# Kernel tuning notes

Hardware: AMD Instinct MI355X
Metric: run time of the kernel (lower is better)

The kernel has to match this reference:

```python
import jax, jax.numpy as jnp
import numpy as np

NF, NLOC, NALL, NNEI = 2, 2048, 3072, 128
Q_DIM = K_DIM = V_DIM = 256
H, D = 8, 32  # num_heads, head_dim
TOTAL = H * D


def setup_inputs() -> dict:
    key = jax.random.key(0)
    ks = jax.random.split(key, 12)
    inp = {
        "q": jax.random.normal(ks[0], (NF, NLOC, Q_DIM), jnp.float32),
        "k": jax.random.normal(ks[1], (NF, NALL, K_DIM), jnp.float32),
        "v": jax.random.normal(ks[2], (NF, NALL, V_DIM), jnp.float32),
        "nlist": jax.random.randint(ks[3], (NF, NLOC, NNEI), 0, NALL, jnp.int64),
        "bias": jax.random.normal(ks[4], (NF, H, NLOC, NNEI), jnp.float32),
        # torch Linear weights: [out, in]
        "Wq": jax.random.normal(ks[5], (TOTAL, Q_DIM), jnp.float32) * 0.05,
        "Wk": jax.random.normal(ks[6], (TOTAL, K_DIM), jnp.float32) * 0.05,
        "Wv": jax.random.normal(ks[7], (TOTAL, V_DIM), jnp.float32) * 0.05,
        "Wg": jax.random.normal(ks[8], (TOTAL, Q_DIM), jnp.float32) * 0.05,
        "bg": jnp.ones((TOTAL,), jnp.float32),  # gating init: bias=1
        "Wo": jax.random.normal(ks[9], (Q_DIM, TOTAL), jnp.float32) * 0.05,
        "bo": jnp.zeros((Q_DIM,), jnp.float32),
    }
    return inp


def reference(q, k, v, nlist, bias, Wq, Wk, Wv, Wg, bg, Wo, bo):
    nf, nloc, _ = q.shape
    nnei = nlist.shape[-1]
    norm = D ** (-0.5)

    g = q @ Wg.T + bg                       # [nf, nloc, TOTAL]
    qh = (q @ Wq.T) * norm                  # [nf, nloc, TOTAL]
    kh = k @ Wk.T                           # [nf, nall, TOTAL]
    vh = v @ Wv.T                           # [nf, nall, TOTAL]

    # gather neighbors: [nf, nloc, nnei, TOTAL]
    fidx = jnp.arange(nf)[:, None, None]
    kg = kh[fidx, nlist].reshape(nf, nloc, nnei, H, D)
    vg = vh[fidx, nlist].reshape(nf, nloc, nnei, H, D)
    qh = qh.reshape(nf, nloc, H, D)

    # per-atom attention: single query vs nnei neighbors
    attn = jnp.einsum("fnhd,fnihd->fhni", qh, kg)      # [nf, H, nloc, nnei]
    attn = jax.nn.softmax(attn + bias, axis=-1)
    o = jnp.einsum("fhni,fnihd->fnhd", attn, vg)       # [nf, nloc, H, D]
    o = o.reshape(nf, nloc, TOTAL)

    o = jax.nn.sigmoid(g) * o
    return o @ Wo.T + bo
```

## Files before the change

### kernel.cpp

```cpp
#include <hip/hip_runtime.h>

#define NF_   2
#define NLOC_ 2048
#define NALL_ 3072
#define NNEI_ 128
#define H_    8
#define D_    32
#define CH_   256

typedef __attribute__((ext_vector_type(8))) short  short8v;
typedef __attribute__((ext_vector_type(8))) unsigned short ushort8v;
typedef __attribute__((ext_vector_type(4))) float  floatx4;

__device__ __forceinline__ unsigned short f2bf(float x) {
  unsigned u = __float_as_uint(x);
  unsigned r = u + 0x7fff + ((u >> 16) & 1);
  return (unsigned short)(r >> 16);
}
__device__ __forceinline__ float bf2f(unsigned short h) {
  return __uint_as_float(((unsigned)h) << 16);
}

__device__ __forceinline__ void cvt_store(unsigned short* hp, unsigned short* lp,
                                          float4 u, float4 v) {
  ushort8v hv, lv;
  hv[0] = f2bf(u.x); lv[0] = f2bf(u.x - bf2f(hv[0]));
  hv[1] = f2bf(u.y); lv[1] = f2bf(u.y - bf2f(hv[1]));
  hv[2] = f2bf(u.z); lv[2] = f2bf(u.z - bf2f(hv[2]));
  hv[3] = f2bf(u.w); lv[3] = f2bf(u.w - bf2f(hv[3]));
  hv[4] = f2bf(v.x); lv[4] = f2bf(v.x - bf2f(hv[4]));
  hv[5] = f2bf(v.y); lv[5] = f2bf(v.y - bf2f(hv[5]));
  hv[6] = f2bf(v.z); lv[6] = f2bf(v.z - bf2f(hv[6]));
  hv[7] = f2bf(v.w); lv[7] = f2bf(v.w - bf2f(hv[7]));
  *(ushort8v*)hp = hv;
  *(ushort8v*)lp = lv;
}

__device__ __forceinline__ void gemm_mfma(
    const float* __restrict__ A, const float* __restrict__ W,
    const float* __restrict__ bvec, float* __restrict__ C,
    int M, int mode,
    unsigned short (*Ah)[40], unsigned short (*Al)[40],
    unsigned short (*Wh)[40], unsigned short (*Wl)[40]) {
  const int t  = threadIdx.x;
  const int m0 = blockIdx.y * 128;
  if (m0 >= M) return;
  const int n0 = blockIdx.x * 128;

  const int lane = t & 63;
  const int wv   = t >> 6;
  const int wr   = wv >> 1;
  const int wc   = wv & 1;
  const int l15  = lane & 15;
  const int ko   = (lane >> 4) * 8;

  const int sr = t >> 1;
  const int sk = (t & 1) * 16;

  floatx4 acc[4][4] = {};

  for (int k0 = 0; k0 < 256; k0 += 32) {
    const float* Ap = A + (size_t)(m0 + sr) * 256 + k0 + sk;
    const float* Wp = W + (size_t)(n0 + sr) * 256 + k0 + sk;
    const float4 a0 = *(const float4*)(Ap + 0);
    const float4 a1 = *(const float4*)(Ap + 4);
    const float4 a2 = *(const float4*)(Ap + 8);
    const float4 a3 = *(const float4*)(Ap + 12);
    const float4 w0 = *(const float4*)(Wp + 0);
    const float4 w1 = *(const float4*)(Wp + 4);
    const float4 w2 = *(const float4*)(Wp + 8);
    const float4 w3 = *(const float4*)(Wp + 12);
    __syncthreads();
    cvt_store(&Ah[sr][sk + 0], &Al[sr][sk + 0], a0, a1);
    cvt_store(&Ah[sr][sk + 8], &Al[sr][sk + 8], a2, a3);
    cvt_store(&Wh[sr][sk + 0], &Wl[sr][sk + 0], w0, w1);
    cvt_store(&Wh[sr][sk + 8], &Wl[sr][sk + 8], w2, w3);
    __syncthreads();

    short8v afh[4], afl[4], bfh[4], bfl[4];
#pragma unroll
    for (int mi = 0; mi < 4; ++mi) {
      const int rr = wr * 64 + mi * 16 + l15;
      afh[mi] = *(const short8v*)&Ah[rr][ko];
      afl[mi] = *(const short8v*)&Al[rr][ko];
    }
#pragma unroll
    for (int ni = 0; ni < 4; ++ni) {
      const int rr = wc * 64 + ni * 16 + l15;
      bfh[ni] = *(const short8v*)&Wh[rr][ko];
      bfl[ni] = *(const short8v*)&Wl[rr][ko];
    }
#pragma unroll
    for (int mi = 0; mi < 4; ++mi)
#pragma unroll
      for (int ni = 0; ni < 4; ++ni) {
        acc[mi][ni] = __builtin_amdgcn_mfma_f32_16x16x32_bf16(
            afh[mi], bfh[ni], acc[mi][ni], 0, 0, 0);
        acc[mi][ni] = __builtin_amdgcn_mfma_f32_16x16x32_bf16(
            afh[mi], bfl[ni], acc[mi][ni], 0, 0, 0);
        acc[mi][ni] = __builtin_amdgcn_mfma_f32_16x16x32_bf16(
            afl[mi], bfh[ni], acc[mi][ni], 0, 0, 0);
      }
  }

  const float norm = 0.17677669529663687f;
#pragma unroll
  for (int mi = 0; mi < 4; ++mi)
#pragma unroll
    for (int ni = 0; ni < 4; ++ni) {
      const int col = n0 + wc * 64 + ni * 16 + l15;
      const float bv = (mode == 1 || mode == 3) ? bvec[col] : 0.f;
#pragma unroll
      for (int r = 0; r < 4; ++r) {
        const int row = m0 + wr * 64 + mi * 16 + (lane >> 4) * 4 + r;
        float vv = acc[mi][ni][r];
        if (mode == 0)      vv *= norm;
        else if (mode == 1) vv = 1.f / (1.f + __expf(-(vv + bv)));
        else if (mode == 3) vv += bv;
        C[(size_t)row * 256 + col] = vv;
      }
    }
}

__global__ __launch_bounds__(256, 2) void proj_kernel(
    const float* __restrict__ q, const float* __restrict__ k, const float* __restrict__ v,
    const float* __restrict__ Wq, const float* __restrict__ Wg,
    const float* __restrict__ Wk, const float* __restrict__ Wv,
    const float* __restrict__ bg,
    float* __restrict__ qh, float* __restrict__ gs,
    float* __restrict__ kh, float* __restrict__ vh) {
  __shared__ unsigned short Ah[128][40], Al[128][40], Wh[128][40], Wl[128][40];
  switch (blockIdx.z) {
    case 0:  gemm_mfma(q, Wq, nullptr, qh, NF_ * NLOC_, 0, Ah, Al, Wh, Wl); break;
    case 1:  gemm_mfma(q, Wg, bg,      gs, NF_ * NLOC_, 1, Ah, Al, Wh, Wl); break;
    case 2:  gemm_mfma(k, Wk, nullptr, kh, NF_ * NALL_, 2, Ah, Al, Wh, Wl); break;
    default: gemm_mfma(v, Wv, nullptr, vh, NF_ * NALL_, 2, Ah, Al, Wh, Wl); break;
  }
}

__global__ __launch_bounds__(256, 2) void out_gemm_kernel(
    const float* __restrict__ x, const float* __restrict__ Wo,
    const float* __restrict__ bo, float* __restrict__ out) {
  __shared__ unsigned short Ah[128][40], Al[128][40], Wh[128][40], Wl[128][40];
  gemm_mfma(x, Wo, bo, out, NF_ * NLOC_, 3, Ah, Al, Wh, Wl);
}

__global__ __launch_bounds__(256, 2) void attn_kernel(
    const float* __restrict__ qh, const float* __restrict__ gs,
    const float* __restrict__ kh, const float* __restrict__ vh,
    const void* __restrict__ nlist, const float* __restrict__ bias,
    float* __restrict__ x) {
  __shared__ float q_s[CH_];
  __shared__ int   jn[NNEI_];
  __shared__ float p[H_][NNEI_ + 4];
  __shared__ float K_s[32][256];

  const int t   = threadIdx.x;
  const int bid = blockIdx.x;
  const int f   = bid >> 11;
  const int n   = bid & (NLOC_ - 1);
  const size_t row = (size_t)bid;

  q_s[t] = qh[row * CH_ + t];

  const int* nl32 = (const int*)nlist;
  int odd_or = 0;
#pragma unroll
  for (int w = 1; w < 16; w += 2) odd_or |= nl32[w];
  if (t < NNEI_) {
    if (odd_or == 0) {
      const long long* nl64 = (const long long*)nlist;
      jn[t] = (int)nl64[row * NNEI_ + t];
    } else {
      jn[t] = nl32[row * NNEI_ + t];
    }
  }
  __syncthreads();

  const int h  = t >> 5;
  const int il = t & 31;
  const int w  = t >> 6;
  const int l  = t & 63;

  float4 qv[8];
  {
    const float4* qp = (const float4*)(q_s + h * D_);
#pragma unroll
    for (int i = 0; i < 8; ++i) qv[i] = qp[i];
  }

  const float* kbase = kh + (size_t)f * NALL_ * CH_;
  const float* bb    = bias + (((size_t)f * H_ + h) * NLOC_ + n) * NNEI_;

  float s[4];
#pragma unroll
  for (int c = 0; c < 4; ++c) {
    if (c) __syncthreads();
#pragma unroll
    for (int u = 0; u < 8; ++u) {
      const int r = w * 8 + u;
      const int j = jn[c * 32 + r];
      const float4 kv = *(const float4*)(kbase + (size_t)j * CH_ + l * 4);
      *(float4*)(&K_s[r][(l ^ (r & 7)) * 4]) = kv;
    }
    __syncthreads();
    const int swz = il & 7;
    const float4* krow = (const float4*)(&K_s[il][0]);
    float a = 0.f;
#pragma unroll
    for (int d4 = 0; d4 < 8; ++d4) {
      const float4 kv = krow[(h * 8 + d4) ^ swz];
      a = fmaf(qv[d4].x, kv.x, a);
      a = fmaf(qv[d4].y, kv.y, a);
      a = fmaf(qv[d4].z, kv.z, a);
      a = fmaf(qv[d4].w, kv.w, a);
    }
    s[c] = a + bb[c * 32 + il];
  }

  float m = fmaxf(fmaxf(s[0], s[1]), fmaxf(s[2], s[3]));
#pragma unroll
  for (int off = 16; off >= 1; off >>= 1) m = fmaxf(m, __shfl_xor(m, off));
  float e[4];
  float sum = 0.f;
#pragma unroll
  for (int r = 0; r < 4; ++r) { e[r] = __expf(s[r] - m); sum += e[r]; }
#pragma unroll
  for (int off = 16; off >= 1; off >>= 1) sum += __shfl_xor(sum, off);
  const float inv = 1.f / sum;
#pragma unroll
  for (int r = 0; r < 4; ++r) p[h][il + 32 * r] = e[r] * inv;
  __syncthreads();

  const float* vb = vh + (size_t)f * NALL_ * CH_ + h * D_ + il;
  float ac0 = 0.f, ac1 = 0.f, ac2 = 0.f, ac3 = 0.f;
  for (int i = 0; i < NNEI_; i += 4) {
    const float4 p4 = *(const float4*)(&p[h][i]);
    const int4  j4 = *(const int4*)(&jn[i]);
    ac0 = fmaf(p4.x, vb[(size_t)j4.x * CH_], ac0);
    ac1 = fmaf(p4.y, vb[(size_t)j4.y * CH_], ac1);
    ac2 = fmaf(p4.z, vb[(size_t)j4.z * CH_], ac2);
    ac3 = fmaf(p4.w, vb[(size_t)j4.w * CH_], ac3);
  }
  const float acc = (ac0 + ac1) + (ac2 + ac3);

  const float g = gs[row * CH_ + t];
  x[row * CH_ + t] = g * acc;
}

extern "C" void kernel_launch(void* const* d_in, const int* in_sizes, int n_in,
                              void* d_out, int out_size, void* d_ws, size_t ws_size,
                              hipStream_t stream) {
  const float* q     = (const float*)d_in[0];
  const float* k     = (const float*)d_in[1];
  const float* v     = (const float*)d_in[2];
  const void*  nlist = d_in[3];
  const float* bias  = (const float*)d_in[4];
  const float* Wq    = (const float*)d_in[5];
  const float* Wk    = (const float*)d_in[6];
  const float* Wv    = (const float*)d_in[7];
  const float* Wg    = (const float*)d_in[8];
  const float* bg    = (const float*)d_in[9];
  const float* Wo    = (const float*)d_in[10];
  const float* bo    = (const float*)d_in[11];
  float* out = (float*)d_out;

  float* ws = (float*)d_ws;
  float* qh = ws;
  float* gs = qh + (size_t)NF_ * NLOC_ * CH_;
  float* kh = gs + (size_t)NF_ * NLOC_ * CH_;
  float* vh = kh + (size_t)NF_ * NALL_ * CH_;
  float* x  = vh + (size_t)NF_ * NALL_ * CH_;

  proj_kernel<<<dim3(2, 48, 4), 256, 0, stream>>>(q, k, v, Wq, Wg, Wk, Wv, bg,
                                                  qh, gs, kh, vh);
  attn_kernel<<<dim3(NF_ * NLOC_), 256, 0, stream>>>(qh, gs, kh, vh, nlist, bias, x);
  out_gemm_kernel<<<dim3(2, 32), 256, 0, stream>>>(x, Wo, bo, out);
}
```

Before: 190.6 us.

## Pre-split weights to bf16 hi/lo once and halve GEMM N-tile

Adds a small kernel that converts the five weight matrices into bf16 high/low pairs once per call, so the GEMM loops load pre-split weights instead of converting fp32 weights in every tile. The GEMM N-tile shrinks from 128 to 64 columns, doubling the number of blocks in the projection and output launches, and occupancy hints are raised for all kernels. The cost is one extra kernel launch plus more A-tile reloads, since each A row is now converted by twice as many blocks.

```diff
diff --git a/kernel.cpp b/kernel.cpp
--- a/kernel.cpp
+++ b/kernel.cpp
@@ -36,8 +36,27 @@
   *(ushort8v*)lp = lv;
 }
 
+__global__ __launch_bounds__(256) void wcvt_kernel(
+    const float* __restrict__ W0, const float* __restrict__ W1,
+    const float* __restrict__ W2, const float* __restrict__ W3,
+    const float* __restrict__ W4, unsigned short* __restrict__ dst) {
+  const float* srcs[5] = {W0, W1, W2, W3, W4};
+  const float* s = srcs[blockIdx.y];
+  unsigned short* hi = dst + (size_t)blockIdx.y * 2 * 65536;
+  unsigned short* lo = hi + 65536;
+  const int idx = (blockIdx.x * 256 + threadIdx.x) * 4;
+  const float4 v = *(const float4*)(s + idx);
+  unsigned short h0 = f2bf(v.x), h1 = f2bf(v.y), h2 = f2bf(v.z), h3 = f2bf(v.w);
+  ushort4 hv = {h0, h1, h2, h3};
+  ushort4 lv = {f2bf(v.x - bf2f(h0)), f2bf(v.y - bf2f(h1)),
+                f2bf(v.z - bf2f(h2)), f2bf(v.w - bf2f(h3))};
+  *(ushort4*)(hi + idx) = hv;
+  *(ushort4*)(lo + idx) = lv;
+}
+
 __device__ __forceinline__ void gemm_mfma(
-    const float* __restrict__ A, const float* __restrict__ W,
+    const float* __restrict__ A,
+    const unsigned short* __restrict__ Whi, const unsigned short* __restrict__ Wlo,
     const float* __restrict__ bvec, float* __restrict__ C,
     int M, int mode,
     unsigned short (*Ah)[40], unsigned short (*Al)[40],
@@ -45,7 +64,7 @@
   const int t  = threadIdx.x;
   const int m0 = blockIdx.y * 128;
   if (m0 >= M) return;
-  const int n0 = blockIdx.x * 128;
+  const int n0 = blockIdx.x * 64;
 
   const int lane = t & 63;
   const int wv   = t >> 6;
@@ -56,28 +75,28 @@
 
   const int sr = t >> 1;
   const int sk = (t & 1) * 16;
-
-  floatx4 acc[4][4] = {};
+  const int wrow = t >> 2;
+  const int wk   = (t & 3) * 8;
+
+  floatx4 acc[4][2] = {};
 
   for (int k0 = 0; k0 < 256; k0 += 32) {
     const float* Ap = A + (size_t)(m0 + sr) * 256 + k0 + sk;
-    const float* Wp = W + (size_t)(n0 + sr) * 256 + k0 + sk;
     const float4 a0 = *(const float4*)(Ap + 0);
     const float4 a1 = *(const float4*)(Ap + 4);
     const float4 a2 = *(const float4*)(Ap + 8);
     const float4 a3 = *(const float4*)(Ap + 12);
-    const float4 w0 = *(const float4*)(Wp + 0);
-    const float4 w1 = *(const float4*)(Wp + 4);
-    const float4 w2 = *(const float4*)(Wp + 8);
-    const float4 w3 = *(const float4*)(Wp + 12);
+    const size_t woff = (size_t)(n0 + wrow) * 256 + k0 + wk;
+    const uint4 whv = *(const uint4*)(Whi + woff);
+    const uint4 wlv = *(const uint4*)(Wlo + woff);
     __syncthreads();
     cvt_store(&Ah[sr][sk + 0], &Al[sr][sk + 0], a0, a1);
     cvt_store(&Ah[sr][sk + 8], &Al[sr][sk + 8], a2, a3);
-    cvt_store(&Wh[sr][sk + 0], &Wl[sr][sk + 0], w0, w1);
-    cvt_store(&Wh[sr][sk + 8], &Wl[sr][sk + 8], w2, w3);
+    *(uint4*)&Wh[wrow][wk] = whv;
+    *(uint4*)&Wl[wrow][wk] = wlv;
     __syncthreads();
 
-    short8v afh[4], afl[4], bfh[4], bfl[4];
+    short8v afh[4], afl[4], bfh[2], bfl[2];
 #pragma unroll
     for (int mi = 0; mi < 4; ++mi) {
       const int rr = wr * 64 + mi * 16 + l15;
@@ -85,15 +104,15 @@
       afl[mi] = *(const short8v*)&Al[rr][ko];
     }
 #pragma unroll
-    for (int ni = 0; ni < 4; ++ni) {
-      const int rr = wc * 64 + ni * 16 + l15;
+    for (int ni = 0; ni < 2; ++ni) {
+      const int rr = wc * 32 + ni * 16 + l15;
       bfh[ni] = *(const short8v*)&Wh[rr][ko];
       bfl[ni] = *(const short8v*)&Wl[rr][ko];
     }
 #pragma unroll
     for (int mi = 0; mi < 4; ++mi)
 #pragma unroll
-      for (int ni = 0; ni < 4; ++ni) {
+      for (int ni = 0; ni < 2; ++ni) {
         acc[mi][ni] = __builtin_amdgcn_mfma_f32_16x16x32_bf16(
             afh[mi], bfh[ni], acc[mi][ni], 0, 0, 0);
         acc[mi][ni] = __builtin_amdgcn_mfma_f32_16x16x32_bf16(
@@ -107,8 +126,8 @@
 #pragma unroll
   for (int mi = 0; mi < 4; ++mi)
 #pragma unroll
-    for (int ni = 0; ni < 4; ++ni) {
-      const int col = n0 + wc * 64 + ni * 16 + l15;
+    for (int ni = 0; ni < 2; ++ni) {
+      const int col = n0 + wc * 32 + ni * 16 + l15;
       const float bv = (mode == 1 || mode == 3) ? bvec[col] : 0.f;
 #pragma unroll
       for (int r = 0; r < 4; ++r) {
@@ -122,30 +141,32 @@
     }
 }
 
-__global__ __launch_bounds__(256, 2) void proj_kernel(
+__global__ __launch_bounds__(256, 3) void proj_kernel(
     const float* __restrict__ q, const float* __restrict__ k, const float* __restrict__ v,
-    const float* __restrict__ Wq, const float* __restrict__ Wg,
-    const float* __restrict__ Wk, const float* __restrict__ Wv,
-    const float* __restrict__ bg,
+    const unsigned short* __restrict__ whl, const float* __restrict__ bg,
     float* __restrict__ qh, float* __restrict__ gs,
     float* __restrict__ kh, float* __restrict__ vh) {
-  __shared__ unsigned short Ah[128][40], Al[128][40], Wh[128][40], Wl[128][40];
+  __shared__ unsigned short Ah[128][40], Al[128][40], Wh[64][40], Wl[64][40];
+  const unsigned short* Whi = whl + (size_t)blockIdx.z * 2 * 65536;
+  const unsigned short* Wlo = Whi + 65536;
   switch (blockIdx.z) {
-    case 0:  gemm_mfma(q, Wq, nullptr, qh, NF_ * NLOC_, 0, Ah, Al, Wh, Wl); break;
-    case 1:  gemm_mfma(q, Wg, bg,      gs, NF_ * NLOC_, 1, Ah, Al, Wh, Wl); break;
-    case 2:  gemm_mfma(k, Wk, nullptr, kh, NF_ * NALL_, 2, Ah, Al, Wh, Wl); break;
-    default: gemm_mfma(v, Wv, nullptr, vh, NF_ * NALL_, 2, Ah, Al, Wh, Wl); break;
-  }
-}
-
-__global__ __launch_bounds__(256, 2) void out_gemm_kernel(
-    const float* __restrict__ x, const float* __restrict__ Wo,
+    case 0:  gemm_mfma(q, Whi, Wlo, nullptr, qh, NF_ * NLOC_, 0, Ah, Al, Wh, Wl); break;
+    case 1:  gemm_mfma(q, Whi, Wlo, bg,      gs, NF_ * NLOC_, 1, Ah, Al, Wh, Wl); break;
+    case 2:  gemm_mfma(k, Whi, Wlo, nullptr, kh, NF_ * NALL_, 2, Ah, Al, Wh, Wl); break;
+    default: gemm_mfma(v, Whi, Wlo, nullptr, vh, NF_ * NALL_, 2, Ah, Al, Wh, Wl); break;
+  }
+}
+
+__global__ __launch_bounds__(256, 3) void out_gemm_kernel(
+    const float* __restrict__ x, const unsigned short* __restrict__ whl,
     const float* __restrict__ bo, float* __restrict__ out) {
-  __shared__ unsigned short Ah[128][40], Al[128][40], Wh[128][40], Wl[128][40];
-  gemm_mfma(x, Wo, bo, out, NF_ * NLOC_, 3, Ah, Al, Wh, Wl);
-}
-
-__global__ __launch_bounds__(256, 2) void attn_kernel(
+  __shared__ unsigned short Ah[128][40], Al[128][40], Wh[64][40], Wl[64][40];
+  const unsigned short* Whi = whl + (size_t)4 * 2 * 65536;
+  const unsigned short* Wlo = Whi + 65536;
+  gemm_mfma(x, Whi, Wlo, bo, out, NF_ * NLOC_, 3, Ah, Al, Wh, Wl);
+}
+
+__global__ __launch_bounds__(256, 4) void attn_kernel(
     const float* __restrict__ qh, const float* __restrict__ gs,
     const float* __restrict__ kh, const float* __restrict__ vh,
     const void* __restrict__ nlist, const float* __restrict__ bias,
@@ -271,9 +292,11 @@
   float* kh = gs + (size_t)NF_ * NLOC_ * CH_;
   float* vh = kh + (size_t)NF_ * NALL_ * CH_;
   float* x  = vh + (size_t)NF_ * NALL_ * CH_;
-
-  proj_kernel<<<dim3(2, 48, 4), 256, 0, stream>>>(q, k, v, Wq, Wg, Wk, Wv, bg,
+  unsigned short* whl = (unsigned short*)(x + (size_t)NF_ * NLOC_ * CH_);
+
+  wcvt_kernel<<<dim3(64, 5), 256, 0, stream>>>(Wq, Wg, Wk, Wv, Wo, whl);
+  proj_kernel<<<dim3(4, 48, 4), 256, 0, stream>>>(q, k, v, whl, bg,
                                                   qh, gs, kh, vh);
   attn_kernel<<<dim3(NF_ * NLOC_), 256, 0, stream>>>(qh, gs, kh, vh, nlist, bias, x);
-  out_gemm_kernel<<<dim3(2, 32), 256, 0, stream>>>(x, Wo, bo, out);
-}
+  out_gemm_kernel<<<dim3(4, 32), 256, 0, stream>>>(x, whl, bo, out);
+}
```

New measurement: 185.3 us. -2.8%, faster.
